# Kernel optimization log

Hardware: AMD Instinct MI355X
Metric: run time of the kernel (lower is better)

The kernel has to match this reference:

```python
import jax, jax.numpy as jnp
import numpy as np
from jax.scipy.special import gammaln

# ---- constants matching init_kwargs ----
D = 64            # num_nodes
K = 64            # DiBS latent rank (k = d default)
P = 32            # n_particles
N_MC = 16         # MC graph samples for score-function grad estimator
PROJ = 128        # proj_dims
N = 2048          # observations
H = 5.0           # h_latent (Frobenius squared-exponential kernel bandwidth)
ALPHA = 0.2       # alpha_linear * t  (single SVGD step)
STEP = 0.005      # SVGD step size
ALPHA_MU = 1.0
ALPHA_LAMBD = float(D + 2)
THETA_MU = 0.0
P_EDGE = 4.0 / (D - 1)          # Erdos-Renyi edge prob (~2 expected edges/node)
LATENT_STD = 1.0 / np.sqrt(K)   # DiBS default latent prior std


def bge_log_marginal(g, data, mu0, alpha_mu, alpha_lambd):
    """BGe log marginal likelihood log p(data | G) for 0/1 adjacency g [d,d]."""
    n, d = data.shape
    small_t = alpha_mu * (alpha_lambd - d - 1.0) / (alpha_mu + 1.0)
    xbar = data.mean(0)
    xc = data - xbar
    R = small_t * jnp.eye(d) + xc.T @ xc \
        + (n * alpha_mu / (n + alpha_mu)) * jnp.outer(xbar - mu0, xbar - mu0)

    def masked_slogdet(mask):  # logdet of R restricted to mask-selected rows/cols
        m = jnp.outer(mask, mask)
        return jnp.linalg.slogdet(m * R + (1.0 - m) * jnp.eye(d))[1]

    def node_score(j):
        parents = g[:, j].astype(R.dtype)
        pj = jnp.maximum(parents, (jnp.arange(d) == j).astype(R.dtype))
        l = jnp.sum(parents)
        log_gamma = (0.5 * (jnp.log(alpha_mu) - jnp.log(n + alpha_mu))
                     + gammaln(0.5 * (n + alpha_lambd - d + l + 1.0))
                     - gammaln(0.5 * (alpha_lambd - d + l + 1.0))
                     - 0.5 * n * jnp.log(jnp.pi)
                     + 0.5 * (alpha_lambd - d + 2.0 * l + 1.0) * jnp.log(small_t))
        return (log_gamma
                + 0.5 * (n + alpha_lambd - d + l) * masked_slogdet(parents)
                - 0.5 * (n + alpha_lambd - d + l + 1.0) * masked_slogdet(pj))

    return jnp.sum(jax.vmap(node_score)(jnp.arange(d)))


def _dense(key, fan_in, fan_out):
    return jax.random.normal(key, (fan_in, fan_out), jnp.float32) * 0.05


def setup_inputs() -> dict:
    key = jax.random.key(0)
    ks = jax.random.split(key, 16)
    return {
        "z_gt": jax.random.normal(ks[0], (N, D), jnp.float32),
        "init_particles_z": jax.random.normal(ks[1], (P, D, K, 2), jnp.float32) * LATENT_STD,
        "enc_w0": _dense(ks[2], D * D, 20), "enc_b0": jnp.zeros(20, jnp.float32),
        "enc_w1": _dense(ks[3], 20, D),     "enc_b1": jnp.zeros(D, jnp.float32),
        "enc_w2": _dense(ks[4], D, D),      "enc_b2": jnp.zeros(D, jnp.float32),
        "mu_w0": _dense(ks[5], D, D), "mu_b0": jnp.zeros(D, jnp.float32),
        "mu_w1": _dense(ks[6], D, D), "mu_b1": jnp.zeros(D, jnp.float32),
        "lv_w0": _dense(ks[7], D, D), "lv_b0": jnp.zeros(D, jnp.float32),
        "lv_w1": _dense(ks[8], D, D), "lv_b1": jnp.zeros(D, jnp.float32),
        "dec_w0": _dense(ks[9], D, 10),       "dec_b0": jnp.zeros(10, jnp.float32),
        "dec_w1": _dense(ks[10], 10, PROJ),   "dec_b1": jnp.zeros(PROJ, jnp.float32),
        "dec_w2": _dense(ks[11], PROJ, PROJ), "dec_b2": jnp.zeros(PROJ, jnp.float32),
        "seed": 0,
    }


def reference(z_gt, init_particles_z, enc_w0, enc_b0, enc_w1, enc_b1, enc_w2, enc_b2,
              mu_w0, mu_b0, mu_w1, mu_b1, lv_w0, lv_b0, lv_w1, lv_b1,
              dec_w0, dec_b0, dec_w1, dec_b1, dec_w2, dec_b2, seed):
    key = jax.random.key(seed)
    d = z_gt.shape[1]
    od = 1.0 - jnp.eye(d)
    z = init_particles_z                                   # [P,d,k,2]
    u, v = z[..., 0], z[..., 1]
    scores = jnp.einsum('pik,pjk->pij', u, v)              # [P,d,d]
    probs = jax.nn.sigmoid(ALPHA * scores) * od            # soft graph, zero diag

    # --- score-function estimate of grad_z log E_G[p(data|G)] (DiBS marginal) ---
    key, sk = jax.random.split(key)
    gs = jax.random.bernoulli(sk, probs[:, None], (P, N_MC, d, d)).astype(z.dtype) * od
    mu0_inf = jnp.zeros(d, z.dtype)
    logp = jax.vmap(jax.vmap(
        lambda g: bge_log_marginal(g, z_gt, mu0_inf, 1.0, d + 2.0)))(gs)   # [P,S]
    w = jax.nn.softmax(logp, axis=1)                       # self-normalized weights
    M = ALPHA * (gs - probs[:, None]) * od                 # d log q(G|Z) / d scores
    grad_u = jnp.einsum('ps,psij,pjk->pik', w, M, v)
    grad_v = jnp.einsum('ps,psij,pik->pjk', w, M, u)

    # --- grad of soft-graph ER prior + Gaussian latent prior ---
    logit_pe = jnp.log(P_EDGE) - jnp.log1p(-P_EDGE)
    Mp = ALPHA * probs * (1.0 - probs) * logit_pe * od
    grad_u = grad_u + jnp.einsum('pij,pjk->pik', Mp, v) - u / (LATENT_STD ** 2)
    grad_v = grad_v + jnp.einsum('pij,pik->pjk', Mp, u) - v / (LATENT_STD ** 2)
    grads = jnp.stack([grad_u, grad_v], axis=-1)           # [P,d,k,2]

    # --- one SVGD step with Frobenius squared-exponential kernel ---
    zf = z.reshape(P, -1)
    gf = grads.reshape(P, -1)
    sq = jnp.sum((zf[:, None] - zf[None]) ** 2, -1)
    Kmat = jnp.exp(-sq / H)                                # symmetric [P,P]
    rep = (-2.0 / H) * (Kmat @ zf - zf * Kmat.sum(1, keepdims=True))
    z_new = z + STEP * ((Kmat @ gf + rep) / P).reshape(z.shape)

    # --- hard graphs: particle_to_g_lim (alpha -> inf) ---
    s2 = jnp.einsum('pik,pjk->pij', z_new[..., 0], z_new[..., 1])
    g_hard = (s2 > 0).astype(z.dtype) * od                 # [P,d,d]

    mu0_bge = jnp.full(d, THETA_MU, z.dtype)
    log_p_z_given_g = jax.vmap(
        lambda g: bge_log_marginal(g, z_gt, mu0_bge, ALPHA_MU, ALPHA_LAMBD))(g_hard)

    # --- q(z | G) encoder (batched over particles) ---
    gf2 = g_hard.reshape(g_hard.shape[0], d * d)
    h = jax.nn.relu(gf2 @ enc_w0 + enc_b0)
    h = jax.nn.relu(h @ enc_w1 + enc_b1)
    h = jax.nn.relu(h @ enc_w2 + enc_b2)
    q_mu = jax.nn.relu(h @ mu_w0 + mu_b0) @ mu_w1 + mu_b1
    q_lv = jax.nn.relu(h @ lv_w0 + lv_b0) @ lv_w1 + lv_b1

    key, rk = jax.random.split(key)
    eps = jax.random.normal(rk, q_lv.shape, q_lv.dtype)
    q_z = q_mu + eps * jnp.exp(0.5 * q_lv)                 # reparameterize

    # --- decoder ---
    hdec = jax.nn.relu(q_z @ dec_w0 + dec_b0)
    hdec = jax.nn.relu(hdec @ dec_w1 + dec_b1)
    recons = hdec @ dec_w2 + dec_b2                        # [P, PROJ]

    return recons, log_p_z_given_g, q_z, q_mu, q_lv, g_hard, z_new
```

## Files before the change

### kernel.cpp

```cpp
#include <hip/hip_runtime.h>
#include <stdint.h>
#include <math.h>

typedef unsigned long long u64;
typedef unsigned int u32;
typedef unsigned short u16;

#define C_P 32
#define C_S 16
#define C_D 64
#define C_N 2048

#define R_OFF      0
#define CTAB_OFF   4160
#define KEYS_OFF   4224
#define PROBS_OFF  4232
#define GROW_OFF   135304
#define GCOL_OFF   168072
#define NS_OFF     200840
#define W_OFF      233608
#define GF_OFF     234120
#define KM_OFF     365192
#define ZN_OFF     365704
#define NS2_OFF    496776

#define O_REC   0
#define O_LOGP  4096
#define O_QZ    4128
#define O_QMU   6176
#define O_QLV   8224
#define O_GH    10272
#define O_ZN    141344
#define O_TOTAL 403488

__device__ __forceinline__ void tf2x32(u32 k0, u32 k1, u32 x0, u32 x1,
                                       u32& o0, u32& o1) {
  u32 ks2 = k0 ^ k1 ^ 0x1BD11BDAu;
  x0 += k0; x1 += k1;
#define TFR(r) { x0 += x1; x1 = (x1 << r) | (x1 >> (32 - r)); x1 ^= x0; }
  TFR(13) TFR(15) TFR(26) TFR(6)   x0 += k1;  x1 += ks2 + 1u;
  TFR(17) TFR(29) TFR(16) TFR(24)  x0 += ks2; x1 += k0 + 2u;
  TFR(13) TFR(15) TFR(26) TFR(6)   x0 += k0;  x1 += k1 + 3u;
  TFR(17) TFR(29) TFR(16) TFR(24)  x0 += k1;  x1 += ks2 + 4u;
  TFR(13) TFR(15) TFR(26) TFR(6)   x0 += ks2; x1 += k0 + 5u;
#undef TFR
  o0 = x0; o1 = x1;
}

__device__ __forceinline__ double d_erfinv(double x) {
  double w = -log1p(-x * x);
  double p;
  if (w < 5.0) {
    w -= 2.5;
    p = 2.81022636e-08;
    p = 3.43273939e-07  + p * w;
    p = -3.5233877e-06  + p * w;
    p = -4.39150654e-06 + p * w;
    p = 0.00021858087   + p * w;
    p = -0.00125372503  + p * w;
    p = -0.00417768164  + p * w;
    p = 0.246640727     + p * w;
    p = 1.50140941      + p * w;
  } else {
    w = sqrt(w) - 3.0;
    p = -0.000200214257;
    p = 0.000100950558  + p * w;
    p = 0.00134934322   + p * w;
    p = -0.00367342844  + p * w;
    p = 0.00573950773   + p * w;
    p = -0.0076224613   + p * w;
    p = 0.00943887047   + p * w;
    p = 1.00167406      + p * w;
    p = 2.83297682      + p * w;
  }
  return p * x;
}

__global__ void k_R(const float* x, double* ws, const int* seedp) {
  __shared__ double pS[8][64], pX[8][64];
  __shared__ double xbar[64];
  int j = blockIdx.x, t = threadIdx.x;
  int i = t & 63, c = t >> 6;
  if (j == 0) {
    if (t < 64) {
      double l = (double)t;
      ws[CTAB_OFF + t] = -0.5 * log(2049.0)
                       + lgamma(0.5 * (2051.0 + l))
                       - lgamma(0.5 * (3.0 + l))
                       - 1024.0 * log(3.14159265358979323846)
                       + 0.5 * (2.0 * l + 3.0) * log(0.5);
    }
    if (t == 0) {
      u32 kk0 = 0u, kk1 = (u32)seedp[0];
      u32 a0, a1, s0, s1, r0, r1, d0, d1;
      tf2x32(kk0, kk1, 0u, 0u, a0, a1);
      tf2x32(kk0, kk1, 0u, 1u, s0, s1);
      tf2x32(a0, a1, 0u, 0u, d0, d1); (void)d0; (void)d1;
      tf2x32(a0, a1, 0u, 1u, r0, r1);
      u32* keys = (u32*)(ws + KEYS_OFF);
      keys[0] = s0; keys[1] = s1; keys[2] = r0; keys[3] = r1;
    }
  }
  double sx = 0.0, sxx = 0.0;
  for (int n = c * 256; n < (c + 1) * 256; n++) {
    double xi = (double)x[n * 64 + i];
    double xj = (double)x[n * 64 + j];
    sx += xi; sxx += xi * xj;
  }
  pS[c][i] = sx; pX[c][i] = sxx;
  __syncthreads();
  if (t < 64) {
    double S = 0.0, X = 0.0;
    for (int cc = 0; cc < 8; cc++) { S += pS[cc][i]; X += pX[cc][i]; }
    xbar[i] = S / 2048.0;
    pX[0][i] = X;
  }
  __syncthreads();
  if (t < 64) {
    double xbi = xbar[i], xbj = xbar[j];
    double s = pX[0][i] - 2048.0 * xbi * xbj + (2048.0 / 2049.0) * xbi * xbj;
    if (i == j) s += 0.5;
    ((float*)(ws + R_OFF))[i * 64 + j] = (float)s;
  }
}

__global__ __launch_bounds__(64) void k_probs(const float* z, double* ws) {
  float* probs = (float*)(ws + PROBS_OFF);
  int b = blockIdx.x; int p = b >> 6, i = b & 63;
  int j = threadIdx.x;
  __shared__ float V[64 * 65];
  __shared__ float us[64];
  int k = j;
  us[k] = z[((p * 64 + i) * 64 + k) * 2 + 0];
  for (int jj = 0; jj < 64; jj++)
    V[jj * 65 + k] = z[((p * 64 + jj) * 64 + k) * 2 + 1];
  __syncthreads();
  float s = 0.f;
  for (int kk = 0; kk < 64; kk++)
    s += us[kk] * V[j * 65 + kk];
  float pr = (i == j) ? 0.f : 1.f / (1.f + expf(-0.2f * s));
  probs[(p * 64 + i) * 64 + j] = pr;
}

__global__ void k_sample(double* ws) {
  const float* probs = (const float*)(ws + PROBS_OFF);
  const u32* keys = (const u32*)(ws + KEYS_OFF);
  u64* grow = (u64*)(ws + GROW_OFF);
  u64* gcol = (u64*)(ws + GCOL_OFF);
  int ps = blockIdx.x;
  int p = ps >> 4;
  int j = threadIdx.x;
  u32 k0 = keys[0], k1 = keys[1];
  u64 colmask = 0;
  for (int i = 0; i < 64; i++) {
    u32 lin = (u32)(ps * 4096 + i * 64 + j);
    u32 o0, o1; tf2x32(k0, k1, 0u, lin, o0, o1);
    u32 bits = o0 ^ o1;
    float f = __uint_as_float((bits >> 9) | 0x3f800000u) - 1.0f;
    bool bit = (f < probs[(p * 64 + i) * 64 + j]);
    u64 rm = __ballot(bit);
    if (j == 0) grow[ps * 64 + i] = rm;
    if (bit) colmask |= (1ull << i);
  }
  gcol[ps * 64 + j] = colmask;
}

__device__ __forceinline__ float rdlane(float x, int l) {
  return __uint_as_float(__builtin_amdgcn_readlane(__float_as_uint(x), (u32)l));
}

template<bool TRANSPOSE>
__global__ __launch_bounds__(64) void k_chol(const float* Rf, const double* ctab,
                                             const u64* masks, double* nodescore) {
  __shared__ float T[2080];
  __shared__ int idx[64];
  int task = blockIdx.x;
  int j = task & 63;
  int lane = threadIdx.x;
  u64 mask;
  if (TRANSPOSE) {
    int p = task >> 6;
    u64 rm = masks[p * 64 + lane];
    mask = __ballot((rm >> j) & 1ull);
  } else {
    mask = masks[task];
  }
  int P = (int)__popcll(mask);
  int m = P + 1;
  u64 below = mask & ((1ull << lane) - 1ull);
  if ((mask >> lane) & 1ull) idx[(int)__popcll(below)] = lane;
  if (lane == 0) idx[P] = j;
  __syncthreads();
  int trLane = (lane * (lane + 1)) >> 1;
  if (lane < m) {
    int cidx = idx[lane];
    int tr = 0;
    for (int r = 0; r < m; r++) {
      if (lane <= r) T[tr + lane] = Rf[idx[r] * 64 + cidx];
      tr += r + 1;
    }
  }
  __syncthreads();
  float mypiv = 1.0f, lastd = 1.0f;
  float v[40];
#pragma unroll
  for (int c = 0; c < 40; c++)
    v[c] = T[trLane + c];
#pragma unroll
  for (int k = 0; k < 40; k++) {
    if (k < m) {
      float dk = rdlane(v[k], k);
      if (lane == k) mypiv = dk;
      lastd = dk;
      float ns = -v[k] * __builtin_amdgcn_rcpf(dk);
#pragma unroll
      for (int b = k + 1; b < 40; b++)
        v[b] += ns * rdlane(v[k], b);
    }
  }
  if (m > 40) {
    for (int b = 40; b < m; b++) {
      float acc = 0.f;
#pragma unroll
      for (int k = 0; k < 40; k++) {
        float dk = rdlane(v[k], k);
        float abk = rdlane(v[k], b);
        acc += v[k] * abk * __builtin_amdgcn_rcpf(dk);
      }
      if (lane >= b) T[trLane + b] -= acc;
    }
    __syncthreads();
    for (int k = 40; k < m; k++) {
      float dk = T[((k * (k + 1)) >> 1) + k];
      if (lane == k) mypiv = dk;
      lastd = dk;
      float sk = T[trLane + k] * __builtin_amdgcn_rcpf(dk);
      for (int b = k + 1; b < m; b++) {
        float abk = T[((b * (b + 1)) >> 1) + k];
        if (lane >= b) T[trLane + b] -= sk * abk;
      }
      __syncthreads();
    }
  }
  double vv = (lane < m) ? log((double)mypiv) : 0.0;
  for (int off = 32; off > 0; off >>= 1) vv += __shfl_down(vv, off, 64);
  if (lane == 0) {
    double logB = vv;
    double logA = logB - log((double)lastd);
    double l = (double)P;
    nodescore[task] = ctab[P]
                    + 0.5 * (2050.0 + l) * logA
                    - 0.5 * (2051.0 + l) * logB;
  }
}

__global__ void k_logpw(const double* ns, double* w) {
  int p = blockIdx.x, t = threadIdx.x;
  __shared__ double part[64];
  int s = t & 15, c = t >> 4;
  double acc = 0.0;
  for (int j = c * 16; j < (c + 1) * 16; j++)
    acc += ns[(p * 16 + s) * 64 + j];
  part[t] = acc;
  __syncthreads();
  if (t < 16) part[t] = part[t] + part[t + 16] + part[t + 32] + part[t + 48];
  __syncthreads();
  if (t == 0) {
    double m = part[0];
    for (int s2 = 1; s2 < 16; s2++) m = fmax(m, part[s2]);
    double e[16], sum = 0.0;
    for (int s2 = 0; s2 < 16; s2++) { e[s2] = exp(part[s2] - m); sum += e[s2]; }
    for (int s2 = 0; s2 < 16; s2++) w[p * 16 + s2] = e[s2] / sum;
  }
}

__global__ void k_grad(double* ws, const float* z) {
  const float* probs = (const float*)(ws + PROBS_OFF);
  const double* w = ws + W_OFF;
  const u64* grow = (const u64*)(ws + GROW_OFF);
  const u64* gcol = (const u64*)(ws + GCOL_OFF);
  float* gf = (float*)(ws + GF_OFF);
  const float LOGIT = -2.6903717578966254f;
  int bb = blockIdx.x;
  int k = threadIdx.x;
  __shared__ float acc[64];
  if (bb < 2048) {
    int p = bb >> 6, i = bb & 63;
    float gb = 0.f, wsum = 0.f;
    for (int s = 0; s < 16; s++) {
      float wv = (float)w[p * 16 + s];
      wsum += wv;
      gb += wv * (float)((grow[(p * 16 + s) * 64 + i] >> k) & 1ull);
    }
    float pr = probs[(p * 64 + i) * 64 + k];
    float od = (i == k) ? 0.f : 1.f;
    acc[k] = (0.2f * (gb - pr * wsum) + 0.2f * pr * (1.f - pr) * LOGIT) * od;
    __syncthreads();
    float s = 0.f;
    for (int j = 0; j < 64; j++)
      s += acc[j] * z[((p * 64 + j) * 64 + k) * 2 + 1];
    s -= 64.f * z[((p * 64 + i) * 64 + k) * 2 + 0];
    gf[p * 8192 + (i * 64 + k) * 2 + 0] = s;
  } else if (bb < 4096) {
    int b = bb - 2048;
    int p = b >> 6, j = b & 63;
    float gb = 0.f, wsum = 0.f;
    for (int s = 0; s < 16; s++) {
      float wv = (float)w[p * 16 + s];
      wsum += wv;
      gb += wv * (float)((gcol[(p * 16 + s) * 64 + j] >> k) & 1ull);
    }
    float pr = probs[(p * 64 + k) * 64 + j];
    float od = (k == j) ? 0.f : 1.f;
    acc[k] = (0.2f * (gb - pr * wsum) + 0.2f * pr * (1.f - pr) * LOGIT) * od;
    __syncthreads();
    float s = 0.f;
    for (int i = 0; i < 64; i++)
      s += acc[i] * z[((p * 64 + i) * 64 + k) * 2 + 0];
    s -= 64.f * z[((p * 64 + j) * 64 + k) * 2 + 1];
    gf[p * 8192 + (j * 64 + k) * 2 + 1] = s;
  } else {
    float* Km = (float*)(ws + KM_OFF);
    int b = bb - 4096;
    int a = b >> 5, b2 = b & 31;
    float accf = 0.f;
    for (int d0 = k; d0 < 8192; d0 += 64) {
      float diff = z[a * 8192 + d0] - z[b2 * 8192 + d0];
      accf += diff * diff;
    }
    for (int off = 32; off > 0; off >>= 1) accf += __shfl_down(accf, off, 64);
    if (k == 0) Km[a * 32 + b2] = expf(-accf / 5.0f);
  }
}

__global__ void k_znew(const float* z, double* ws, float* out) {
  const float* Km = (const float*)(ws + KM_OFF);
  const float* gf = (const float*)(ws + GF_OFF);
  float* zn = (float*)(ws + ZN_OFF);
  int gid = blockIdx.x * 64 + threadIdx.x;
  int p = gid >> 13, t = gid & 8191;
  float zp = z[p * 8192 + t];
  float accg = 0.f, accz = 0.f, ks = 0.f;
  for (int b = 0; b < 32; b++) {
    float kv = Km[p * 32 + b];
    accg += kv * gf[b * 8192 + t];
    accz += kv * z[b * 8192 + t];
    ks += kv;
  }
  float rep = -0.4f * (accz - zp * ks);
  float v = zp + 0.005f * ((accg + rep) / 32.f);
  zn[p * 8192 + t] = v;
  out[O_ZN + p * 8192 + t] = v;
}

__global__ __launch_bounds__(64) void k_s2col(double* ws, float* out) {
  const float* zn = (const float*)(ws + ZN_OFF);
  u64* grow2 = (u64*)(ws + NS_OFF);
  int b = blockIdx.x; int p = b >> 6, i = b & 63;
  int j = threadIdx.x;
  __shared__ float V[64 * 65];
  __shared__ float us[64];
  int k = j;
  us[k] = zn[p * 8192 + (i * 64 + k) * 2 + 0];
  for (int jj = 0; jj < 64; jj++)
    V[jj * 65 + k] = zn[p * 8192 + (jj * 64 + k) * 2 + 1];
  __syncthreads();
  float s = 0.f;
  for (int kk = 0; kk < 64; kk++)
    s += us[kk] * V[j * 65 + kk];
  bool bit = (i != j) && (s > 0.0f);
  out[O_GH + (p * 64 + i) * 64 + j] = bit ? 1.0f : 0.0f;
  u64 m = __ballot(bit);
  if (j == 0) grow2[p * 64 + i] = m;
}

__global__ void k_mlp(double* ws, float* out, const double* ns2,
    const float* ew0, const float* eb0, const float* ew1, const float* eb1,
    const float* ew2, const float* eb2,
    const float* mw0, const float* mb0, const float* mw1, const float* mb1,
    const float* lw0, const float* lb0, const float* lw1, const float* lb1,
    const float* dw0, const float* db0, const float* dw1, const float* db1,
    const float* dw2, const float* db2) {
  int p = blockIdx.x, t = threadIdx.x;
  const u64* grow2 = (const u64*)(ws + NS_OFF);
  const u32* keys = (const u32*)(ws + KEYS_OFF);
  __shared__ float part[64][20];
  __shared__ float h0[20], h1[64], h2[64], hm[64], hl[64];
  __shared__ float qmu[64], qlv[64], qz[64], h3[10], h4[128];
  __shared__ u64 gc[64];
  {
    double vv = ns2[p * 64 + t];
    for (int off = 32; off > 0; off >>= 1) vv += __shfl_down(vv, off, 64);
    if (t == 0) out[O_LOGP + p] = (float)vv;
  }
  {
    u64 cmask = 0;
    for (int i = 0; i < 64; i++)
      cmask |= ((grow2[p * 64 + i] >> t) & 1ull) << i;
    gc[t] = cmask;
  }
  __syncthreads();
  {
    float acc[20];
#pragma unroll
    for (int o = 0; o < 20; o++) acc[o] = 0.f;
    u64 m = gc[t];
    for (int i = 0; i < 64; i++) {
      float msk = (float)((m >> i) & 1ull);
      const float* wr = ew0 + (i * 64 + t) * 20;
#pragma unroll
      for (int o = 0; o < 20; o++) acc[o] += msk * wr[o];
    }
    for (int o = 0; o < 20; o++) part[t][o] = acc[o];
  }
  __syncthreads();
  if (t < 20) {
    float s = eb0[t];
    for (int q = 0; q < 64; q++) s += part[q][t];
    h0[t] = fmaxf(s, 0.f);
  }
  __syncthreads();
  {
    float s = eb1[t];
    for (int q = 0; q < 20; q++) s += h0[q] * ew1[q * 64 + t];
    h1[t] = fmaxf(s, 0.f);
  }
  __syncthreads();
  {
    float s = eb2[t];
    for (int q = 0; q < 64; q++) s += h1[q] * ew2[q * 64 + t];
    h2[t] = fmaxf(s, 0.f);
  }
  __syncthreads();
  {
    float s = mb0[t];
    for (int q = 0; q < 64; q++) s += h2[q] * mw0[q * 64 + t];
    hm[t] = fmaxf(s, 0.f);
    float s2 = lb0[t];
    for (int q = 0; q < 64; q++) s2 += h2[q] * lw0[q * 64 + t];
    hl[t] = fmaxf(s2, 0.f);
  }
  __syncthreads();
  {
    float s = mb1[t];
    for (int q = 0; q < 64; q++) s += hm[q] * mw1[q * 64 + t];
    qmu[t] = s;
    float s2 = lb1[t];
    for (int q = 0; q < 64; q++) s2 += hl[q] * lw1[q * 64 + t];
    qlv[t] = s2;
  }
  {
    u32 o0, o1;
    tf2x32(keys[2], keys[3], 0u, (u32)(p * 64 + t), o0, o1);
    u32 bits = o0 ^ o1;
    float f = __uint_as_float((bits >> 9) | 0x3f800000u) - 1.0f;
    float LOF = __uint_as_float(0xBF7FFFFFu);
    float uu = fmaxf(LOF, f * 2.0f + LOF);
    float eps = (float)(1.4142135623730951 * d_erfinv((double)uu));
    float qzv = qmu[t] + eps * expf(0.5f * qlv[t]);
    qz[t] = qzv;
    out[O_QZ  + p * 64 + t] = qzv;
    out[O_QMU + p * 64 + t] = qmu[t];
    out[O_QLV + p * 64 + t] = qlv[t];
  }
  __syncthreads();
  if (t < 10) {
    float s = db0[t];
    for (int q = 0; q < 64; q++) s += qz[q] * dw0[q * 10 + t];
    h3[t] = fmaxf(s, 0.f);
  }
  __syncthreads();
  for (int o = t; o < 128; o += 64) {
    float s = db1[o];
    for (int q = 0; q < 10; q++) s += h3[q] * dw1[q * 128 + o];
    h4[o] = fmaxf(s, 0.f);
  }
  __syncthreads();
  for (int o = t; o < 128; o += 64) {
    float s = db2[o];
    for (int q = 0; q < 128; q++) s += h4[q] * dw2[q * 128 + o];
    out[O_REC + p * 128 + o] = s;
  }
}

extern "C" void kernel_launch(void* const* d_in, const int* in_sizes, int n_in,
                              void* d_out, int out_size, void* d_ws, size_t ws_size,
                              hipStream_t stream) {
  (void)in_sizes; (void)n_in; (void)out_size; (void)ws_size;
  const float* z_gt = (const float*)d_in[0];
  const float* z0   = (const float*)d_in[1];
  const float* ew0 = (const float*)d_in[2];  const float* eb0 = (const float*)d_in[3];
  const float* ew1 = (const float*)d_in[4];  const float* eb1 = (const float*)d_in[5];
  const float* ew2 = (const float*)d_in[6];  const float* eb2 = (const float*)d_in[7];
  const float* mw0 = (const float*)d_in[8];  const float* mb0 = (const float*)d_in[9];
  const float* mw1 = (const float*)d_in[10]; const float* mb1 = (const float*)d_in[11];
  const float* lw0 = (const float*)d_in[12]; const float* lb0 = (const float*)d_in[13];
  const float* lw1 = (const float*)d_in[14]; const float* lb1 = (const float*)d_in[15];
  const float* dw0 = (const float*)d_in[16]; const float* db0 = (const float*)d_in[17];
  const float* dw1 = (const float*)d_in[18]; const float* db1 = (const float*)d_in[19];
  const float* dw2 = (const float*)d_in[20]; const float* db2 = (const float*)d_in[21];
  const int* seed = (const int*)d_in[22];
  double* ws = (double*)d_ws;
  float* out = (float*)d_out;
  const float* Rf = (const float*)(ws + R_OFF);

  k_R<<<64, 512, 0, stream>>>(z_gt, ws, seed);
  k_probs<<<C_P * C_D, 64, 0, stream>>>(z0, ws);
  k_sample<<<C_P * C_S, 64, 0, stream>>>(ws);
  k_chol<false><<<C_P * C_S * C_D, 64, 0, stream>>>(Rf, ws + CTAB_OFF,
      (const u64*)(ws + GCOL_OFF), ws + NS_OFF);
  k_logpw<<<C_P, 64, 0, stream>>>(ws + NS_OFF, ws + W_OFF);
  k_grad<<<2 * C_P * C_D + C_P * C_P, 64, 0, stream>>>(ws, z0);
  k_znew<<<(C_P * 8192) / 64, 64, 0, stream>>>(z0, ws, out);
  k_s2col<<<C_P * C_D, 64, 0, stream>>>(ws, out);
  k_chol<true><<<C_P * C_D, 64, 0, stream>>>(Rf, ws + CTAB_OFF,
      (const u64*)(ws + NS_OFF), ws + NS2_OFF);
  k_mlp<<<C_P, 64, 0, stream>>>(ws, out, ws + NS2_OFF,
      ew0, eb0, ew1, eb1, ew2, eb2,
      mw0, mb0, mw1, mb1, lw0, lb0, lw1, lb1,
      dw0, db0, dw1, db1, dw2, db2);
}
```

Measured before the change: 380.6 us.

## Fuse R/probs kernels, fold logpw into grad, add small-m Cholesky path

```diff
diff --git a/kernel.cpp b/kernel.cpp
--- a/kernel.cpp
+++ b/kernel.cpp
@@ -18,7 +18,6 @@
 #define GROW_OFF   135304
 #define GCOL_OFF   168072
 #define NS_OFF     200840
-#define W_OFF      233608
 #define GF_OFF     234120
 #define KM_OFF     365192
 #define ZN_OFF     365704
@@ -76,70 +75,75 @@
   return p * x;
 }
 
-__global__ void k_R(const float* x, double* ws, const int* seedp) {
+__global__ __launch_bounds__(512) void k_Rprobs(const float* x, const float* z,
+                                                double* ws, const int* seedp) {
   __shared__ double pS[8][64], pX[8][64];
   __shared__ double xbar[64];
-  int j = blockIdx.x, t = threadIdx.x;
-  int i = t & 63, c = t >> 6;
-  if (j == 0) {
+  __shared__ float V[64 * 65];
+  __shared__ float us[8][64];
+  int blk = blockIdx.x, t = threadIdx.x;
+  if (blk < 64) {
+    int j = blk;
+    int i = t & 63, c = t >> 6;
+    if (j == 0) {
+      if (t < 64) {
+        double l = (double)t;
+        ws[CTAB_OFF + t] = -0.5 * log(2049.0)
+                         + lgamma(0.5 * (2051.0 + l))
+                         - lgamma(0.5 * (3.0 + l))
+                         - 1024.0 * log(3.14159265358979323846)
+                         + 0.5 * (2.0 * l + 3.0) * log(0.5);
+      }
+      if (t == 0) {
+        u32 kk0 = 0u, kk1 = (u32)seedp[0];
+        u32 a0, a1, s0, s1, r0, r1, d0, d1;
+        tf2x32(kk0, kk1, 0u, 0u, a0, a1);
+        tf2x32(kk0, kk1, 0u, 1u, s0, s1);
+        tf2x32(a0, a1, 0u, 0u, d0, d1); (void)d0; (void)d1;
+        tf2x32(a0, a1, 0u, 1u, r0, r1);
+        u32* keys = (u32*)(ws + KEYS_OFF);
+        keys[0] = s0; keys[1] = s1; keys[2] = r0; keys[3] = r1;
+      }
+    }
+    double sx = 0.0, sxx = 0.0;
+    for (int n = c * 256; n < (c + 1) * 256; n++) {
+      double xi = (double)x[n * 64 + i];
+      double xj = (double)x[n * 64 + j];
+      sx += xi; sxx += xi * xj;
+    }
+    pS[c][i] = sx; pX[c][i] = sxx;
+    __syncthreads();
     if (t < 64) {
-      double l = (double)t;
-      ws[CTAB_OFF + t] = -0.5 * log(2049.0)
-                       + lgamma(0.5 * (2051.0 + l))
-                       - lgamma(0.5 * (3.0 + l))
-                       - 1024.0 * log(3.14159265358979323846)
-                       + 0.5 * (2.0 * l + 3.0) * log(0.5);
-    }
-    if (t == 0) {
-      u32 kk0 = 0u, kk1 = (u32)seedp[0];
-      u32 a0, a1, s0, s1, r0, r1, d0, d1;
-      tf2x32(kk0, kk1, 0u, 0u, a0, a1);
-      tf2x32(kk0, kk1, 0u, 1u, s0, s1);
-      tf2x32(a0, a1, 0u, 0u, d0, d1); (void)d0; (void)d1;
-      tf2x32(a0, a1, 0u, 1u, r0, r1);
-      u32* keys = (u32*)(ws + KEYS_OFF);
-      keys[0] = s0; keys[1] = s1; keys[2] = r0; keys[3] = r1;
-    }
-  }
-  double sx = 0.0, sxx = 0.0;
-  for (int n = c * 256; n < (c + 1) * 256; n++) {
-    double xi = (double)x[n * 64 + i];
-    double xj = (double)x[n * 64 + j];
-    sx += xi; sxx += xi * xj;
-  }
-  pS[c][i] = sx; pX[c][i] = sxx;
-  __syncthreads();
-  if (t < 64) {
-    double S = 0.0, X = 0.0;
-    for (int cc = 0; cc < 8; cc++) { S += pS[cc][i]; X += pX[cc][i]; }
-    xbar[i] = S / 2048.0;
-    pX[0][i] = X;
-  }
-  __syncthreads();
-  if (t < 64) {
-    double xbi = xbar[i], xbj = xbar[j];
-    double s = pX[0][i] - 2048.0 * xbi * xbj + (2048.0 / 2049.0) * xbi * xbj;
-    if (i == j) s += 0.5;
-    ((float*)(ws + R_OFF))[i * 64 + j] = (float)s;
-  }
-}
-
-__global__ __launch_bounds__(64) void k_probs(const float* z, double* ws) {
-  float* probs = (float*)(ws + PROBS_OFF);
-  int b = blockIdx.x; int p = b >> 6, i = b & 63;
-  int j = threadIdx.x;
-  __shared__ float V[64 * 65];
-  __shared__ float us[64];
-  int k = j;
-  us[k] = z[((p * 64 + i) * 64 + k) * 2 + 0];
-  for (int jj = 0; jj < 64; jj++)
-    V[jj * 65 + k] = z[((p * 64 + jj) * 64 + k) * 2 + 1];
-  __syncthreads();
-  float s = 0.f;
-  for (int kk = 0; kk < 64; kk++)
-    s += us[kk] * V[j * 65 + kk];
-  float pr = (i == j) ? 0.f : 1.f / (1.f + expf(-0.2f * s));
-  probs[(p * 64 + i) * 64 + j] = pr;
+      double S = 0.0, X = 0.0;
+      for (int cc = 0; cc < 8; cc++) { S += pS[cc][i]; X += pX[cc][i]; }
+      xbar[i] = S / 2048.0;
+      pX[0][i] = X;
+    }
+    __syncthreads();
+    if (t < 64) {
+      double xbi = xbar[i], xbj = xbar[j];
+      double s = pX[0][i] - 2048.0 * xbi * xbj + (2048.0 / 2049.0) * xbi * xbj;
+      if (i == j) s += 0.5;
+      ((float*)(ws + R_OFF))[i * 64 + j] = (float)s;
+    }
+  } else {
+    int b = blk - 64;
+    int p = b >> 3, ig = b & 7;
+    int w = t >> 6, k = t & 63;
+    int i = ig * 8 + w;
+    for (int q = 0; q < 8; q++) {
+      int jj = w * 8 + q;
+      V[jj * 65 + k] = z[((p * 64 + jj) * 64 + k) * 2 + 1];
+    }
+    us[w][k] = z[((p * 64 + i) * 64 + k) * 2 + 0];
+    __syncthreads();
+    int j = k;
+    float s = 0.f;
+    for (int kk = 0; kk < 64; kk++)
+      s += us[w][kk] * V[j * 65 + kk];
+    float pr = (i == j) ? 0.f : 1.f / (1.f + expf(-0.2f * s));
+    ((float*)(ws + PROBS_OFF))[(p * 64 + i) * 64 + j] = pr;
+  }
 }
 
 __global__ void k_sample(double* ws) {
@@ -202,44 +206,63 @@
   }
   __syncthreads();
   float mypiv = 1.0f, lastd = 1.0f;
-  float v[40];
-#pragma unroll
-  for (int c = 0; c < 40; c++)
-    v[c] = T[trLane + c];
-#pragma unroll
-  for (int k = 0; k < 40; k++) {
-    if (k < m) {
-      float dk = rdlane(v[k], k);
-      if (lane == k) mypiv = dk;
-      lastd = dk;
-      float ns = -v[k] * __builtin_amdgcn_rcpf(dk);
-#pragma unroll
-      for (int b = k + 1; b < 40; b++)
-        v[b] += ns * rdlane(v[k], b);
-    }
-  }
-  if (m > 40) {
-    for (int b = 40; b < m; b++) {
-      float acc = 0.f;
-#pragma unroll
-      for (int k = 0; k < 40; k++) {
+  if (m <= 32) {
+    float v[32];
+#pragma unroll
+    for (int c = 0; c < 32; c++)
+      v[c] = T[trLane + c];
+#pragma unroll
+    for (int k = 0; k < 32; k++) {
+      if (k < m) {
         float dk = rdlane(v[k], k);
-        float abk = rdlane(v[k], b);
-        acc += v[k] * abk * __builtin_amdgcn_rcpf(dk);
-      }
-      if (lane >= b) T[trLane + b] -= acc;
-    }
-    __syncthreads();
-    for (int k = 40; k < m; k++) {
-      float dk = T[((k * (k + 1)) >> 1) + k];
-      if (lane == k) mypiv = dk;
-      lastd = dk;
-      float sk = T[trLane + k] * __builtin_amdgcn_rcpf(dk);
-      for (int b = k + 1; b < m; b++) {
-        float abk = T[((b * (b + 1)) >> 1) + k];
-        if (lane >= b) T[trLane + b] -= sk * abk;
-      }
-      __syncthreads();
+        if (lane == k) mypiv = dk;
+        lastd = dk;
+        float ns = -v[k] * __builtin_amdgcn_rcpf(dk);
+#pragma unroll
+        for (int b = k + 1; b < 32; b++)
+          v[b] += ns * rdlane(v[k], b);
+      }
+    }
+  } else {
+    float v[40];
+#pragma unroll
+    for (int c = 0; c < 40; c++)
+      v[c] = T[trLane + c];
+#pragma unroll
+    for (int k = 0; k < 40; k++) {
+      if (k < m) {
+        float dk = rdlane(v[k], k);
+        if (lane == k) mypiv = dk;
+        lastd = dk;
+        float ns = -v[k] * __builtin_amdgcn_rcpf(dk);
+#pragma unroll
+        for (int b = k + 1; b < 40; b++)
+          v[b] += ns * rdlane(v[k], b);
+      }
+    }
+    if (m > 40) {
+      for (int b = 40; b < m; b++) {
+        float acc = 0.f;
+#pragma unroll
+        for (int k = 0; k < 40; k++) {
+          float dk = rdlane(v[k], k);
+          float abk = rdlane(v[k], b);
+          acc += v[k] * abk * __builtin_amdgcn_rcpf(dk);
+        }
+        if (lane >= b) T[trLane + b] -= acc;
+      }
+      __syncthreads();
+      for (int k = 40; k < m; k++) {
+        float dk = T[((k * (k + 1)) >> 1) + k];
+        if (lane == k) mypiv = dk;
+        lastd = dk;
+        float sk = T[trLane + k] * __builtin_amdgcn_rcpf(dk);
+        for (int b = k + 1; b < m; b++) {
+          float abk = T[((b * (b + 1)) >> 1) + k];
+          if (lane >= b) T[trLane + b] -= sk * abk;
+        }
+        __syncthreads();
+      }
     }
   }
   double vv = (lane < m) ? log((double)mypiv) : 0.0;
@@ -254,29 +277,9 @@
   }
 }
 
-__global__ void k_logpw(const double* ns, double* w) {
-  int p = blockIdx.x, t = threadIdx.x;
-  __shared__ double part[64];
-  int s = t & 15, c = t >> 4;
-  double acc = 0.0;
-  for (int j = c * 16; j < (c + 1) * 16; j++)
-    acc += ns[(p * 16 + s) * 64 + j];
-  part[t] = acc;
-  __syncthreads();
-  if (t < 16) part[t] = part[t] + part[t + 16] + part[t + 32] + part[t + 48];
-  __syncthreads();
-  if (t == 0) {
-    double m = part[0];
-    for (int s2 = 1; s2 < 16; s2++) m = fmax(m, part[s2]);
-    double e[16], sum = 0.0;
-    for (int s2 = 0; s2 < 16; s2++) { e[s2] = exp(part[s2] - m); sum += e[s2]; }
-    for (int s2 = 0; s2 < 16; s2++) w[p * 16 + s2] = e[s2] / sum;
-  }
-}
-
 __global__ void k_grad(double* ws, const float* z) {
   const float* probs = (const float*)(ws + PROBS_OFF);
-  const double* w = ws + W_OFF;
+  const double* ns = ws + NS_OFF;
   const u64* grow = (const u64*)(ws + GROW_OFF);
   const u64* gcol = (const u64*)(ws + GCOL_OFF);
   float* gf = (float*)(ws + GF_OFF);
@@ -284,41 +287,69 @@
   int bb = blockIdx.x;
   int k = threadIdx.x;
   __shared__ float acc[64];
-  if (bb < 2048) {
-    int p = bb >> 6, i = bb & 63;
-    float gb = 0.f, wsum = 0.f;
-    for (int s = 0; s < 16; s++) {
-      float wv = (float)w[p * 16 + s];
-      wsum += wv;
-      gb += wv * (float)((grow[(p * 16 + s) * 64 + i] >> k) & 1ull);
-    }
-    float pr = probs[(p * 64 + i) * 64 + k];
-    float od = (i == k) ? 0.f : 1.f;
-    acc[k] = (0.2f * (gb - pr * wsum) + 0.2f * pr * (1.f - pr) * LOGIT) * od;
-    __syncthreads();
-    float s = 0.f;
-    for (int j = 0; j < 64; j++)
-      s += acc[j] * z[((p * 64 + j) * 64 + k) * 2 + 1];
-    s -= 64.f * z[((p * 64 + i) * 64 + k) * 2 + 0];
-    gf[p * 8192 + (i * 64 + k) * 2 + 0] = s;
-  } else if (bb < 4096) {
-    int b = bb - 2048;
-    int p = b >> 6, j = b & 63;
-    float gb = 0.f, wsum = 0.f;
-    for (int s = 0; s < 16; s++) {
-      float wv = (float)w[p * 16 + s];
-      wsum += wv;
-      gb += wv * (float)((gcol[(p * 16 + s) * 64 + j] >> k) & 1ull);
-    }
-    float pr = probs[(p * 64 + k) * 64 + j];
-    float od = (k == j) ? 0.f : 1.f;
-    acc[k] = (0.2f * (gb - pr * wsum) + 0.2f * pr * (1.f - pr) * LOGIT) * od;
-    __syncthreads();
-    float s = 0.f;
-    for (int i = 0; i < 64; i++)
-      s += acc[i] * z[((p * 64 + i) * 64 + k) * 2 + 0];
-    s -= 64.f * z[((p * 64 + j) * 64 + k) * 2 + 1];
-    gf[p * 8192 + (j * 64 + k) * 2 + 1] = s;
+  __shared__ double part[64];
+  __shared__ double lp[16];
+  __shared__ double ebuf[16];
+  __shared__ float wbuf[16];
+  if (bb < 4096) {
+    int p = (bb < 2048) ? (bb >> 6) : ((bb - 2048) >> 6);
+    {
+      int s = k & 15, c = k >> 4;
+      double a = 0.0;
+      for (int jj = c * 16; jj < c * 16 + 16; jj++)
+        a += ns[(p * 16 + s) * 64 + jj];
+      part[k] = a;
+      __syncthreads();
+      if (k < 16) lp[k] = part[k] + part[k + 16] + part[k + 32] + part[k + 48];
+      __syncthreads();
+      if (k < 16) {
+        double mx = lp[0];
+        for (int s2 = 1; s2 < 16; s2++) mx = fmax(mx, lp[s2]);
+        ebuf[k] = exp(lp[k] - mx);
+      }
+      __syncthreads();
+      if (k < 16) {
+        double sum = 0.0;
+        for (int s2 = 0; s2 < 16; s2++) sum += ebuf[s2];
+        wbuf[k] = (float)(ebuf[k] / sum);
+      }
+      __syncthreads();
+    }
+    if (bb < 2048) {
+      int i = bb & 63;
+      float gb = 0.f, wsum = 0.f;
+      for (int s = 0; s < 16; s++) {
+        float wv = wbuf[s];
+        wsum += wv;
+        gb += wv * (float)((grow[(p * 16 + s) * 64 + i] >> k) & 1ull);
+      }
+      float pr = probs[(p * 64 + i) * 64 + k];
+      float od = (i == k) ? 0.f : 1.f;
+      acc[k] = (0.2f * (gb - pr * wsum) + 0.2f * pr * (1.f - pr) * LOGIT) * od;
+      __syncthreads();
+      float s = 0.f;
+      for (int jj = 0; jj < 64; jj++)
+        s += acc[jj] * z[((p * 64 + jj) * 64 + k) * 2 + 1];
+      s -= 64.f * z[((p * 64 + i) * 64 + k) * 2 + 0];
+      gf[p * 8192 + (i * 64 + k) * 2 + 0] = s;
+    } else {
+      int jcol = (bb - 2048) & 63;
+      float gb = 0.f, wsum = 0.f;
+      for (int s = 0; s < 16; s++) {
+        float wv = wbuf[s];
+        wsum += wv;
+        gb += wv * (float)((gcol[(p * 16 + s) * 64 + jcol] >> k) & 1ull);
+      }
+      float pr = probs[(p * 64 + k) * 64 + jcol];
+      float od = (k == jcol) ? 0.f : 1.f;
+      acc[k] = (0.2f * (gb - pr * wsum) + 0.2f * pr * (1.f - pr) * LOGIT) * od;
+      __syncthreads();
+      float s = 0.f;
+      for (int i = 0; i < 64; i++)
+        s += acc[i] * z[((p * 64 + i) * 64 + k) * 2 + 0];
+      s -= 64.f * z[((p * 64 + jcol) * 64 + k) * 2 + 1];
+      gf[p * 8192 + (jcol * 64 + k) * 2 + 1] = s;
+    }
   } else {
     float* Km = (float*)(ws + KM_OFF);
     int b = bb - 4096;
@@ -504,12 +535,10 @@
   float* out = (float*)d_out;
   const float* Rf = (const float*)(ws + R_OFF);
 
-  k_R<<<64, 512, 0, stream>>>(z_gt, ws, seed);
-  k_probs<<<C_P * C_D, 64, 0, stream>>>(z0, ws);
+  k_Rprobs<<<320, 512, 0, stream>>>(z_gt, z0, ws, seed);
   k_sample<<<C_P * C_S, 64, 0, stream>>>(ws);
   k_chol<false><<<C_P * C_S * C_D, 64, 0, stream>>>(Rf, ws + CTAB_OFF,
       (const u64*)(ws + GCOL_OFF), ws + NS_OFF);
-  k_logpw<<<C_P, 64, 0, stream>>>(ws + NS_OFF, ws + W_OFF);
   k_grad<<<2 * C_P * C_D + C_P * C_P, 64, 0, stream>>>(ws, z0);
   k_znew<<<(C_P * 8192) / 64, 64, 0, stream>>>(z0, ws, out);
   k_s2col<<<C_P * C_D, 64, 0, stream>>>(ws, out);
```

New measurement: 388.5 us. +2.1%, slower.
